# Performance work log

Hardware: AMD Instinct MI355X
Metric: run time of the kernel (lower is better)

## Reference

```python
import jax, jax.numpy as jnp
import numpy as np

N_TASKS = 8
D_MODEL = 1024
HIDDEN = 1024
N_CLASSES = 100
BATCH = 8192


def setup_inputs() -> dict:
    key = jax.random.key(0)
    ks = jax.random.split(key, 6)
    s1 = 1.0 / np.sqrt(D_MODEL)
    s2 = 1.0 / np.sqrt(HIDDEN)
    return {
        "x": jax.random.normal(ks[0], (BATCH, D_MODEL), dtype=jnp.float32),
        "task_id": jax.random.randint(ks[1], (BATCH,), 0, N_TASKS),
        "W1": jax.random.uniform(ks[2], (N_TASKS, D_MODEL, HIDDEN), jnp.float32, -s1, s1),
        "b1": jax.random.uniform(ks[3], (N_TASKS, HIDDEN), jnp.float32, -s1, s1),
        "W2": jax.random.uniform(ks[4], (N_TASKS, HIDDEN, N_CLASSES), jnp.float32, -s2, s2),
        "b2": jax.random.uniform(ks[5], (N_TASKS, N_CLASSES), jnp.float32, -s2, s2),
    }


def reference(x, task_id, W1, b1, W2, b2):
    # Per-task 2-layer MLP heads; dropout is identity (inference).
    # Compute all heads batched, then select each row's head via one-hot.
    h = jax.nn.relu(jnp.einsum("bd,tdh->tbh", x, W1) + b1[:, None, :])  # [T,B,H]
    logits = jnp.einsum("tbh,thc->tbc", h, W2) + b2[:, None, :]          # [T,B,C]
    onehot = jax.nn.one_hot(task_id, W1.shape[0], dtype=x.dtype)          # [B,T]
    return jnp.einsum("tbc,bt->bc", logits, onehot)                      # [B,C]
```

## Files before the change

kernel.cpp:

```cpp
#include <hip/hip_runtime.h>
#include <hip/hip_bf16.h>
#include <stdint.h>

#define T_TASKS 8
#define DM      1024
#define HID     1024
#define NC      100
#define NCP     128
#define BATCH   8192
#define MPAD    9216

typedef __bf16 bf16x8 __attribute__((ext_vector_type(8)));
typedef float  f32x4  __attribute__((ext_vector_type(4)));
typedef unsigned int u32;
#define GAS __attribute__((address_space(1)))
#define LAS __attribute__((address_space(3)))

__device__ __forceinline__ unsigned short f2bf(float f) {
  __hip_bfloat16 h = __float2bfloat16(f);
  return __builtin_bit_cast(unsigned short, h);
}

__device__ __forceinline__ float bf2f(unsigned short u) {
  const u32 v = ((u32)u) << 16;
  return __builtin_bit_cast(float, v);
}

__global__ void init_k(int* __restrict__ perm, int* __restrict__ gmeta) {
  const int gid = blockIdx.x * 256 + threadIdx.x;
  const uint4 m1 = {0xFFFFFFFFu, 0xFFFFFFFFu, 0xFFFFFFFFu, 0xFFFFFFFFu};
  uint4* p4 = (uint4*)perm;
  if (gid < MPAD / 4) p4[gid] = m1;
  if (gid < 16) gmeta[gid] = 0;
}

__global__ void count_k(const int* __restrict__ task_id, int* __restrict__ gmeta) {
  __shared__ int h[T_TASKS];
  const int tid = threadIdx.x;
  if (tid < T_TASKS) h[tid] = 0;
  __syncthreads();
  atomicAdd(&h[task_id[blockIdx.x * 256 + tid]], 1);
  __syncthreads();
  if (tid < T_TASKS) atomicAdd(&gmeta[tid], h[tid]);
}

__global__ void scatter_k(const int* __restrict__ task_id, int* __restrict__ gmeta,
                          int* __restrict__ perm, int* __restrict__ starts) {
  __shared__ int h[T_TASKS];
  __shared__ int base[T_TASKS];
  __shared__ int sst[T_TASKS + 1];
  const int tid = threadIdx.x;
  if (tid < T_TASKS) h[tid] = 0;
  if (tid == 0) {
    int off = 0;
    for (int t = 0; t < T_TASKS; ++t) {
      sst[t] = off;
      off += (gmeta[t] + 127) & ~127;
    }
    sst[T_TASKS] = off;
  }
  __syncthreads();
  const int r = blockIdx.x * 256 + tid;
  const int t = task_id[r];
  const int slot = atomicAdd(&h[t], 1);
  __syncthreads();
  if (tid < T_TASKS) base[tid] = atomicAdd(&gmeta[8 + tid], h[tid]);
  __syncthreads();
  perm[sst[t] + base[t] + slot] = r;
  if (blockIdx.x == 0 && tid <= T_TASKS) starts[tid] = sst[tid];
}

__global__ void gather_x(const float* __restrict__ x,
                         const int* __restrict__ perm,
                         unsigned short* __restrict__ XP) {
  const int p = blockIdx.x;
  const int r = perm[p];
  const int c = threadIdx.x * 4;
  ushort4 v;
  if (r >= 0) {
    const float4 f = *(const float4*)(x + (size_t)r * DM + c);
    v.x = f2bf(f.x); v.y = f2bf(f.y); v.z = f2bf(f.z); v.w = f2bf(f.w);
  } else {
    v.x = 0; v.y = 0; v.z = 0; v.w = 0;
  }
  *(ushort4*)(XP + (size_t)p * DM + c) = v;
}

__global__ void transpose_w1(const float* __restrict__ W1,
                             unsigned short* __restrict__ W1T) {
  __shared__ unsigned short tile[64][65];
  const int t  = blockIdx.z;
  const int d0 = blockIdx.x * 64;
  const int h0 = blockIdx.y * 64;
  const int tid = threadIdx.x;
  const float* src = W1 + (size_t)t * DM * HID;
  unsigned short* dst = W1T + (size_t)t * HID * DM;
#pragma unroll
  for (int i = 0; i < 16; ++i) {
    int idx = tid + 256 * i;
    int ld = idx >> 6, lh = idx & 63;
    tile[lh][ld] = f2bf(src[(size_t)(d0 + ld) * HID + h0 + lh]);
  }
  __syncthreads();
#pragma unroll
  for (int i = 0; i < 16; ++i) {
    int idx = tid + 256 * i;
    int lh = idx >> 6, ld = idx & 63;
    dst[(size_t)(h0 + lh) * DM + d0 + ld] = tile[lh][ld];
  }
}

__global__ void transpose_w2_packed(const float* __restrict__ W2,
                                    unsigned short* __restrict__ W2F) {
  __shared__ unsigned short tile[128 * 72];
  const int t  = blockIdx.y;
  const int h0 = blockIdx.x * 64;
  const int tid = threadIdx.x;
  const float* src = W2 + (size_t)t * HID * NC;
#pragma unroll
  for (int i = 0; i < 36; ++i) tile[tid + 256 * i] = 0;
  __syncthreads();
#pragma unroll
  for (int i = 0; i < 32; ++i) {
    const int idx = tid + 256 * i;
    const int row = idx >> 7, col = idx & 127;
    if (col < NC)
      tile[col * 72 + row] = f2bf(src[(size_t)(h0 + row) * NC + col]);
  }
  __syncthreads();
  const int w = tid >> 6, lane = tid & 63;
  const int lr = lane & 15, quad = lane >> 4;
#pragma unroll
  for (int e = 0; e < 4; ++e) {
    const int fi = w * 4 + e;
    const int ci = fi >> 1, kcl = fi & 1;
    const uint4 v = *(const uint4*)&tile[(ci * 16 + lr) * 72 + kcl * 32 + quad * 8];
    unsigned short* dst =
        W2F + (((size_t)t * 8 + ci) * 32 + (h0 >> 5) + kcl) * 512 + lane * 8;
    *(uint4*)dst = v;
  }
}

__global__ __launch_bounds__(256, 2) void gemm_fused4(
    const unsigned short* __restrict__ XP,
    const unsigned short* __restrict__ W1T,
    const unsigned short* __restrict__ W2F,
    const float* __restrict__ b1,
    const int* __restrict__ starts,
    unsigned short* __restrict__ Lp)
{
  __shared__ __align__(16) unsigned short lds[18432];
  unsigned short* As = lds;
  unsigned short* Bs = lds + 8192;
  unsigned short* hS = lds;

  const int tid = threadIdx.x;
  const int p0  = blockIdx.x * 128;
  const int n0  = blockIdx.y * 128;

  if (p0 >= starts[T_TASKS]) return;

  int task = 0;
#pragma unroll
  for (int t = 1; t < T_TASKS; ++t)
    if (p0 >= starts[t]) task = t;

  const int wave = tid >> 6;
  const int lane = tid & 63;
  const int wm   = (wave >> 1) * 64;
  const int wn   = (wave & 1) * 64;
  const int lr   = lane & 15;
  const int quad = lane >> 4;

  const int crow = tid >> 3;
  const int kc   = (tid & 7) ^ (crow & 7);
  const unsigned short* pA[4];
  const unsigned short* pB[4];
  const unsigned short* Bg = W1T + ((size_t)task * HID + n0) * 1024;
#pragma unroll
  for (int i = 0; i < 4; ++i) {
    const int row = crow + 32 * i;
    pA[i] = XP + (size_t)(p0 + row) * 1024 + kc * 8;
    pB[i] = Bg + (size_t)row * 1024 + kc * 8;
  }

  f32x4 acc[4][4];
#pragma unroll
  for (int i = 0; i < 4; ++i)
#pragma unroll
    for (int j = 0; j < 4; ++j) acc[i][j] = (f32x4){0.f, 0.f, 0.f, 0.f};

  const int sw0 = quad ^ (lr & 7);
  const int sw1 = (4 + quad) ^ (lr & 7);

  for (int k0 = 0; k0 < 1024; k0 += 64) {
#pragma unroll
    for (int i = 0; i < 4; ++i) {
      __builtin_amdgcn_global_load_lds((const GAS u32*)(pA[i] + k0),
                                       (LAS u32*)&As[(tid + 256 * i) * 8], 16, 0, 0);
      __builtin_amdgcn_global_load_lds((const GAS u32*)(pB[i] + k0),
                                       (LAS u32*)&Bs[(tid + 256 * i) * 8], 16, 0, 0);
    }
    __syncthreads();
    {
      bf16x8 a[4], b[4];
#pragma unroll
      for (int i = 0; i < 4; ++i)
        a[i] = *(const bf16x8*)&As[((wm + i * 16 + lr) * 8 + sw0) * 8];
#pragma unroll
      for (int j = 0; j < 4; ++j)
        b[j] = *(const bf16x8*)&Bs[((wn + j * 16 + lr) * 8 + sw0) * 8];
#pragma unroll
      for (int i = 0; i < 4; ++i)
#pragma unroll
        for (int j = 0; j < 4; ++j)
          acc[i][j] = __builtin_amdgcn_mfma_f32_16x16x32_bf16(a[i], b[j], acc[i][j], 0, 0, 0);
#pragma unroll
      for (int i = 0; i < 4; ++i)
        a[i] = *(const bf16x8*)&As[((wm + i * 16 + lr) * 8 + sw1) * 8];
#pragma unroll
      for (int j = 0; j < 4; ++j)
        b[j] = *(const bf16x8*)&Bs[((wn + j * 16 + lr) * 8 + sw1) * 8];
#pragma unroll
      for (int i = 0; i < 4; ++i)
#pragma unroll
        for (int j = 0; j < 4; ++j)
          acc[i][j] = __builtin_amdgcn_mfma_f32_16x16x32_bf16(a[i], b[j], acc[i][j], 0, 0, 0);
    }
    __syncthreads();
  }

  float b1v[4];
#pragma unroll
  for (int ni = 0; ni < 4; ++ni)
    b1v[ni] = b1[task * HID + n0 + wn + ni * 16 + lr];
#pragma unroll
  for (int mi = 0; mi < 4; ++mi)
#pragma unroll
    for (int r = 0; r < 4; ++r) {
      const int row = wm + mi * 16 + quad * 4 + r;
#pragma unroll
      for (int ni = 0; ni < 4; ++ni) {
        float v = acc[mi][ni][r] + b1v[ni];
        v = v > 0.f ? v : 0.f;
        hS[row * 136 + wn + ni * 16 + lr] = f2bf(v);
      }
    }
  __syncthreads();

  const int cbase = (wave & 1) * 4;
  const unsigned short* pW2 =
      W2F + (((size_t)task * 8 + cbase) * 32 + blockIdx.y * 4) * 512 + lane * 8;

  f32x4 acc2[4][4];
#pragma unroll
  for (int mi = 0; mi < 4; ++mi)
#pragma unroll
    for (int ci = 0; ci < 4; ++ci) acc2[mi][ci] = (f32x4){0.f, 0.f, 0.f, 0.f};

#pragma unroll
  for (int e = 0; e < 4; ++e) {
    bf16x8 w2p[4], a2[4];
#pragma unroll
    for (int ci = 0; ci < 4; ++ci)
      w2p[ci] = *(const bf16x8*)(pW2 + ((size_t)ci * 32 + e) * 512);
#pragma unroll
    for (int mi = 0; mi < 4; ++mi)
      a2[mi] = *(const bf16x8*)&hS[(wm + mi * 16 + lr) * 136 + e * 32 + quad * 8];
#pragma unroll
    for (int mi = 0; mi < 4; ++mi)
#pragma unroll
      for (int ci = 0; ci < 4; ++ci)
        acc2[mi][ci] = __builtin_amdgcn_mfma_f32_16x16x32_bf16(
            a2[mi], w2p[ci], acc2[mi][ci], 0, 0, 0);
  }

  unsigned short* lp = Lp + ((size_t)blockIdx.y * MPAD + p0) * NCP;
#pragma unroll
  for (int mi = 0; mi < 4; ++mi)
#pragma unroll
    for (int r = 0; r < 4; ++r) {
      const int row = wm + mi * 16 + quad * 4 + r;
#pragma unroll
      for (int ci = 0; ci < 4; ++ci)
        lp[row * NCP + wn + ci * 16 + lr] = f2bf(acc2[mi][ci][r]);
    }
}

__global__ void reduce_k(const unsigned short* __restrict__ Lp,
                         const int* __restrict__ perm,
                         const int* __restrict__ task_id,
                         const float* __restrict__ b2,
                         float* __restrict__ Out) {
  const int gid = blockIdx.x * 256 + threadIdx.x;
  const int row = gid >> 5;
  const int c4  = (gid & 31) * 4;
  if (c4 >= NC) return;
  const int og = perm[row];
  if (og < 0) return;
  float s0 = 0.f, s1 = 0.f, s2 = 0.f, s3 = 0.f;
#pragma unroll
  for (int sp = 0; sp < 8; ++sp) {
    const ushort4 v = *(const ushort4*)(Lp + ((size_t)sp * MPAD + row) * NCP + c4);
    s0 += bf2f(v.x); s1 += bf2f(v.y); s2 += bf2f(v.z); s3 += bf2f(v.w);
  }
  const int task = task_id[og];
  const float4 bb = *(const float4*)(b2 + (size_t)task * NC + c4);
  float4 o;
  o.x = s0 + bb.x; o.y = s1 + bb.y; o.z = s2 + bb.z; o.w = s3 + bb.w;
  *(float4*)(Out + (size_t)og * NC + c4) = o;
}

extern "C" void kernel_launch(void* const* d_in, const int* in_sizes, int n_in,
                              void* d_out, int out_size, void* d_ws, size_t ws_size,
                              hipStream_t stream) {
  const float* x       = (const float*)d_in[0];
  const int*   task_id = (const int*)d_in[1];
  const float* W1      = (const float*)d_in[2];
  const float* b1      = (const float*)d_in[3];
  const float* W2      = (const float*)d_in[4];
  const float* b2      = (const float*)d_in[5];
  float* out = (float*)d_out;

  char* ws = (char*)d_ws;
  int* perm   = (int*)(ws + 0);
  int* gmeta  = (int*)(ws + 36864);
  int* starts = (int*)(ws + 36928);
  unsigned short* XP  = (unsigned short*)(ws + 65536);
  unsigned short* W1T = (unsigned short*)(ws + 18939904);
  unsigned short* W2F = (unsigned short*)(ws + 35717120);
  unsigned short* Lp  = (unsigned short*)(ws + 37814272);

  init_k<<<9, 256, 0, stream>>>(perm, gmeta);
  count_k<<<32, 256, 0, stream>>>(task_id, gmeta);
  scatter_k<<<32, 256, 0, stream>>>(task_id, gmeta, perm, starts);
  gather_x<<<MPAD, 256, 0, stream>>>(x, perm, XP);
  transpose_w1<<<dim3(16, 16, T_TASKS), 256, 0, stream>>>(W1, W1T);
  transpose_w2_packed<<<dim3(16, T_TASKS), 256, 0, stream>>>(W2, W2F);
  gemm_fused4<<<dim3(MPAD / 128, HID / 128), 256, 0, stream>>>(
      XP, W1T, W2F, b1, starts, Lp);
  reduce_k<<<MPAD * 32 / 256, 256, 0, stream>>>(Lp, perm, task_id, b2, out);
}
```

Baseline: 160.4 us.

## Fuse preprocessing kernels and replace global atomics with per-block count prefix

Merges the x gather/convert, the W1 transpose and the W2 pack into one launch that branches on block index. It also removes the init kernel by having count_k clear perm itself and write per-block counts, so scatter_k computes its offsets deterministically from a prefix sum instead of global atomics. The W1 transpose now uses float4 loads and 16-byte stores instead of scalar accesses. The aim is fewer launches and better memory access in the W1 conversion. The cost is a larger, heterogeneous kernel whose shared-memory use is sized for the biggest branch.

New measurement: 153.3 us. 4.4% less time.

```diff
diff --git a/kernel.cpp b/kernel.cpp
--- a/kernel.cpp
+++ b/kernel.cpp
@@ -26,118 +26,140 @@
   return __builtin_bit_cast(float, v);
 }
 
-__global__ void init_k(int* __restrict__ perm, int* __restrict__ gmeta) {
-  const int gid = blockIdx.x * 256 + threadIdx.x;
-  const uint4 m1 = {0xFFFFFFFFu, 0xFFFFFFFFu, 0xFFFFFFFFu, 0xFFFFFFFFu};
-  uint4* p4 = (uint4*)perm;
-  if (gid < MPAD / 4) p4[gid] = m1;
-  if (gid < 16) gmeta[gid] = 0;
-}
-
-__global__ void count_k(const int* __restrict__ task_id, int* __restrict__ gmeta) {
+__global__ void count_k(const int* __restrict__ task_id,
+                        int* __restrict__ gcount, int* __restrict__ perm) {
   __shared__ int h[T_TASKS];
   const int tid = threadIdx.x;
+  const int bx  = blockIdx.x;
   if (tid < T_TASKS) h[tid] = 0;
   __syncthreads();
-  atomicAdd(&h[task_id[blockIdx.x * 256 + tid]], 1);
-  __syncthreads();
-  if (tid < T_TASKS) atomicAdd(&gmeta[tid], h[tid]);
-}
-
-__global__ void scatter_k(const int* __restrict__ task_id, int* __restrict__ gmeta,
+  atomicAdd(&h[task_id[bx * 256 + tid]], 1);
+  const int base = bx * (MPAD / 32);
+  for (int i = tid; i < MPAD / 32; i += 256) perm[base + i] = -1;
+  __syncthreads();
+  if (tid < T_TASKS) gcount[bx * T_TASKS + tid] = h[tid];
+}
+
+__global__ void scatter_k(const int* __restrict__ task_id,
+                          const int* __restrict__ gcount,
                           int* __restrict__ perm, int* __restrict__ starts) {
   __shared__ int h[T_TASKS];
-  __shared__ int base[T_TASKS];
+  __shared__ int tot[T_TASKS], prev[T_TASKS];
   __shared__ int sst[T_TASKS + 1];
   const int tid = threadIdx.x;
-  if (tid < T_TASKS) h[tid] = 0;
+  const int bx  = blockIdx.x;
+  if (tid < T_TASKS) {
+    h[tid] = 0;
+    int s = 0, p = 0;
+    for (int b = 0; b < 32; ++b) {
+      const int c = gcount[b * T_TASKS + tid];
+      s += c;
+      if (b < bx) p += c;
+    }
+    tot[tid] = s; prev[tid] = p;
+  }
+  __syncthreads();
   if (tid == 0) {
     int off = 0;
-    for (int t = 0; t < T_TASKS; ++t) {
-      sst[t] = off;
-      off += (gmeta[t] + 127) & ~127;
-    }
+    for (int t = 0; t < T_TASKS; ++t) { sst[t] = off; off += (tot[t] + 127) & ~127; }
     sst[T_TASKS] = off;
   }
-  __syncthreads();
-  const int r = blockIdx.x * 256 + tid;
+  const int r = bx * 256 + tid;
   const int t = task_id[r];
   const int slot = atomicAdd(&h[t], 1);
   __syncthreads();
-  if (tid < T_TASKS) base[tid] = atomicAdd(&gmeta[8 + tid], h[tid]);
-  __syncthreads();
-  perm[sst[t] + base[t] + slot] = r;
-  if (blockIdx.x == 0 && tid <= T_TASKS) starts[tid] = sst[tid];
-}
-
-__global__ void gather_x(const float* __restrict__ x,
-                         const int* __restrict__ perm,
-                         unsigned short* __restrict__ XP) {
-  const int p = blockIdx.x;
-  const int r = perm[p];
-  const int c = threadIdx.x * 4;
-  ushort4 v;
-  if (r >= 0) {
-    const float4 f = *(const float4*)(x + (size_t)r * DM + c);
-    v.x = f2bf(f.x); v.y = f2bf(f.y); v.z = f2bf(f.z); v.w = f2bf(f.w);
-  } else {
-    v.x = 0; v.y = 0; v.z = 0; v.w = 0;
-  }
-  *(ushort4*)(XP + (size_t)p * DM + c) = v;
-}
-
-__global__ void transpose_w1(const float* __restrict__ W1,
-                             unsigned short* __restrict__ W1T) {
-  __shared__ unsigned short tile[64][65];
-  const int t  = blockIdx.z;
-  const int d0 = blockIdx.x * 64;
-  const int h0 = blockIdx.y * 64;
+  perm[sst[t] + prev[t] + slot] = r;
+  if (bx == 0 && tid <= T_TASKS) starts[tid] = sst[tid];
+}
+
+#define GX_BLKS MPAD
+#define W1_BLKS (T_TASKS * 16 * 16)
+#define W2_BLKS (16 * T_TASKS)
+__global__ void preproc_fused(const float* __restrict__ x,
+                              const int* __restrict__ perm,
+                              unsigned short* __restrict__ XP,
+                              const float* __restrict__ W1,
+                              unsigned short* __restrict__ W1T,
+                              const float* __restrict__ W2,
+                              unsigned short* __restrict__ W2F) {
+  __shared__ unsigned short tile[128 * 72];
+  const int bid = blockIdx.x;
   const int tid = threadIdx.x;
-  const float* src = W1 + (size_t)t * DM * HID;
-  unsigned short* dst = W1T + (size_t)t * HID * DM;
-#pragma unroll
-  for (int i = 0; i < 16; ++i) {
-    int idx = tid + 256 * i;
-    int ld = idx >> 6, lh = idx & 63;
-    tile[lh][ld] = f2bf(src[(size_t)(d0 + ld) * HID + h0 + lh]);
-  }
-  __syncthreads();
-#pragma unroll
-  for (int i = 0; i < 16; ++i) {
-    int idx = tid + 256 * i;
-    int lh = idx >> 6, ld = idx & 63;
-    dst[(size_t)(h0 + lh) * DM + d0 + ld] = tile[lh][ld];
-  }
-}
-
-__global__ void transpose_w2_packed(const float* __restrict__ W2,
-                                    unsigned short* __restrict__ W2F) {
-  __shared__ unsigned short tile[128 * 72];
-  const int t  = blockIdx.y;
-  const int h0 = blockIdx.x * 64;
-  const int tid = threadIdx.x;
-  const float* src = W2 + (size_t)t * HID * NC;
-#pragma unroll
-  for (int i = 0; i < 36; ++i) tile[tid + 256 * i] = 0;
-  __syncthreads();
-#pragma unroll
-  for (int i = 0; i < 32; ++i) {
-    const int idx = tid + 256 * i;
-    const int row = idx >> 7, col = idx & 127;
-    if (col < NC)
-      tile[col * 72 + row] = f2bf(src[(size_t)(h0 + row) * NC + col]);
-  }
-  __syncthreads();
-  const int w = tid >> 6, lane = tid & 63;
-  const int lr = lane & 15, quad = lane >> 4;
-#pragma unroll
-  for (int e = 0; e < 4; ++e) {
-    const int fi = w * 4 + e;
-    const int ci = fi >> 1, kcl = fi & 1;
-    const uint4 v = *(const uint4*)&tile[(ci * 16 + lr) * 72 + kcl * 32 + quad * 8];
-    unsigned short* dst =
-        W2F + (((size_t)t * 8 + ci) * 32 + (h0 >> 5) + kcl) * 512 + lane * 8;
-    *(uint4*)dst = v;
+
+  if (bid < GX_BLKS) {
+    const int r = perm[bid];
+    const int c = tid * 4;
+    ushort4 v;
+    if (r >= 0) {
+      const float4 f = *(const float4*)(x + (size_t)r * DM + c);
+      v.x = f2bf(f.x); v.y = f2bf(f.y); v.z = f2bf(f.z); v.w = f2bf(f.w);
+    } else {
+      v.x = 0; v.y = 0; v.z = 0; v.w = 0;
+    }
+    *(ushort4*)(XP + (size_t)bid * DM + c) = v;
+    return;
+  }
+
+  if (bid < GX_BLKS + W1_BLKS) {
+    const int b  = bid - GX_BLKS;
+    const int t  = b >> 8;
+    const int rem = b & 255;
+    const int d0 = (rem >> 4) * 64;
+    const int h0 = (rem & 15) * 64;
+    const float* src = W1 + (size_t)t * DM * HID;
+    unsigned short* dst = W1T + (size_t)t * HID * DM;
+#pragma unroll
+    for (int i = 0; i < 4; ++i) {
+      const int idx = tid + 256 * i;
+      const int d  = idx >> 4;
+      const int hc = (idx & 15) * 4;
+      const float4 f = *(const float4*)(src + (size_t)(d0 + d) * HID + h0 + hc);
+      tile[(hc + 0) * 65 + d] = f2bf(f.x);
+      tile[(hc + 1) * 65 + d] = f2bf(f.y);
+      tile[(hc + 2) * 65 + d] = f2bf(f.z);
+      tile[(hc + 3) * 65 + d] = f2bf(f.w);
+    }
+    __syncthreads();
+#pragma unroll
+    for (int i = 0; i < 2; ++i) {
+      const int idx = tid + 256 * i;
+      const int lh  = idx >> 3;
+      const int ldc = idx & 7;
+      union { uint4 v; unsigned short s[8]; } o;
+#pragma unroll
+      for (int q = 0; q < 8; ++q) o.s[q] = tile[lh * 65 + ldc * 8 + q];
+      *(uint4*)(dst + (size_t)(h0 + lh) * DM + d0 + ldc * 8) = o.v;
+    }
+    return;
+  }
+
+  {
+    const int b  = bid - (GX_BLKS + W1_BLKS);
+    const int t  = b >> 4;
+    const int h0 = (b & 15) * 64;
+    const float* src = W2 + (size_t)t * HID * NC;
+#pragma unroll
+    for (int i = 0; i < 36; ++i) tile[tid + 256 * i] = 0;
+    __syncthreads();
+#pragma unroll
+    for (int i = 0; i < 32; ++i) {
+      const int idx = tid + 256 * i;
+      const int row = idx >> 7, col = idx & 127;
+      if (col < NC)
+        tile[col * 72 + row] = f2bf(src[(size_t)(h0 + row) * NC + col]);
+    }
+    __syncthreads();
+    const int w = tid >> 6, lane = tid & 63;
+    const int lr = lane & 15, quad = lane >> 4;
+#pragma unroll
+    for (int e = 0; e < 4; ++e) {
+      const int fi = w * 4 + e;
+      const int ci = fi >> 1, kcl = fi & 1;
+      const uint4 v = *(const uint4*)&tile[(ci * 16 + lr) * 72 + kcl * 32 + quad * 8];
+      unsigned short* dstp =
+          W2F + (((size_t)t * 8 + ci) * 32 + (h0 >> 5) + kcl) * 512 + lane * 8;
+      *(uint4*)dstp = v;
+    }
   }
 }
 
@@ -324,19 +346,17 @@
 
   char* ws = (char*)d_ws;
   int* perm   = (int*)(ws + 0);
-  int* gmeta  = (int*)(ws + 36864);
-  int* starts = (int*)(ws + 36928);
+  int* gcount = (int*)(ws + 36864);
+  int* starts = (int*)(ws + 37888);
   unsigned short* XP  = (unsigned short*)(ws + 65536);
   unsigned short* W1T = (unsigned short*)(ws + 18939904);
   unsigned short* W2F = (unsigned short*)(ws + 35717120);
   unsigned short* Lp  = (unsigned short*)(ws + 37814272);
 
-  init_k<<<9, 256, 0, stream>>>(perm, gmeta);
-  count_k<<<32, 256, 0, stream>>>(task_id, gmeta);
-  scatter_k<<<32, 256, 0, stream>>>(task_id, gmeta, perm, starts);
-  gather_x<<<MPAD, 256, 0, stream>>>(x, perm, XP);
-  transpose_w1<<<dim3(16, 16, T_TASKS), 256, 0, stream>>>(W1, W1T);
-  transpose_w2_packed<<<dim3(16, T_TASKS), 256, 0, stream>>>(W2, W2F);
+  count_k<<<32, 256, 0, stream>>>(task_id, gcount, perm);
+  scatter_k<<<32, 256, 0, stream>>>(task_id, gcount, perm, starts);
+  preproc_fused<<<GX_BLKS + W1_BLKS + W2_BLKS, 256, 0, stream>>>(
+      x, perm, XP, W1, W1T, W2, W2F);
   gemm_fused4<<<dim3(MPAD / 128, HID / 128), 256, 0, stream>>>(
       XP, W1T, W2F, b1, starts, Lp);
   reduce_k<<<MPAD * 32 / 256, 256, 0, stream>>>(Lp, perm, task_id, b2, out);
```
